# Kernel optimization log

Hardware: AMD Instinct MI355X
Metric: run time of the kernel (lower is better)

The kernel has to match this reference:

```python
import jax, jax.numpy as jnp
import numpy as np

D = 512  # link/path state dim == GRU hidden
R = 256  # readout dim
T = 8    # message-passing steps


def gru_cell(x, h, W_ih, W_hh, b_ih, b_hh):
    # torch nn.GRU cell math (weights stored [3H, in])
    gi = x @ W_ih.T + b_ih
    gh = h @ W_hh.T + b_hh
    i_r, i_z, i_n = jnp.split(gi, 3, axis=-1)
    h_r, h_z, h_n = jnp.split(gh, 3, axis=-1)
    r = jax.nn.sigmoid(i_r + h_r)
    z = jax.nn.sigmoid(i_z + h_z)
    n = jnp.tanh(i_n + r * h_n)
    return (1.0 - z) * n + z * h


def setup_inputs():
    key = jax.random.key(0)
    n_links, n_paths, L = 2000, 20000, 6
    ks = jax.random.split(key, 24)
    links = jax.random.randint(ks[0], (n_paths * L,), 0, n_links)
    paths = jnp.repeat(jnp.arange(n_paths), L)   # path id per entry
    seqs = jnp.tile(jnp.arange(L), n_paths)      # position of link within path
    link_capacity = jax.random.uniform(ks[1], (n_links, 1))
    bandwidth = jax.random.uniform(ks[2], (n_paths, 1))

    def u(k, shape, fan_in):
        s = 1.0 / np.sqrt(fan_in)
        return jax.random.uniform(k, shape, minval=-s, maxval=s)

    inp = dict(links=links, paths=paths, seqs=seqs,
               link_capacity=link_capacity, bandwidth=bandwidth)
    # path GRU (p_U) and link GRU (l_U)
    inp['Wih_p'] = u(ks[3], (3 * D, D), D); inp['Whh_p'] = u(ks[4], (3 * D, D), D)
    inp['bih_p'] = u(ks[5], (3 * D,), D);   inp['bhh_p'] = u(ks[6], (3 * D,), D)
    inp['Wih_l'] = u(ks[7], (3 * D, D), D); inp['Whh_l'] = u(ks[8], (3 * D, D), D)
    inp['bih_l'] = u(ks[9], (3 * D,), D);   inp['bhh_l'] = u(ks[10], (3 * D,), D)
    # readout MLPs (delay + jitter), torch Linear layout [out, in]
    inp['d_w1'] = u(ks[11], (R, D), D);      inp['d_b1'] = u(ks[12], (R,), D)
    inp['d_w2'] = u(ks[13], (R // 2, R), R); inp['d_b2'] = u(ks[14], (R // 2,), R)
    inp['d_w3'] = u(ks[15], (1, R // 2), R // 2); inp['d_b3'] = u(ks[16], (1,), R // 2)
    inp['j_w1'] = u(ks[17], (R, D), D);      inp['j_b1'] = u(ks[18], (R,), D)
    inp['j_w2'] = u(ks[19], (R // 2, R), R); inp['j_b2'] = u(ks[20], (R // 2,), R)
    inp['j_w3'] = u(ks[21], (1, R // 2), R // 2); inp['j_b3'] = u(ks[22], (1,), R // 2)
    inp['n_links'] = n_links
    inp['n_paths'] = n_paths
    inp['max_seq_len'] = L  # == max(seqs)+1
    return inp


def mlp(x, w1, b1, w2, b2, w3, b3):
    h = jax.nn.relu(x @ w1.T + b1)
    h = jax.nn.relu(h @ w2.T + b2)
    return h @ w3.T + b3


def reference(links, paths, seqs, link_capacity, bandwidth,
              Wih_p, Whh_p, bih_p, bhh_p, Wih_l, Whh_l, bih_l, bhh_l,
              d_w1, d_b1, d_w2, d_b2, d_w3, d_b3,
              j_w1, j_b1, j_w2, j_b2, j_w3, j_b3,
              n_links, n_paths, max_seq_len):
    dt = bandwidth.dtype
    path_h = jnp.concatenate([bandwidth, jnp.zeros((n_paths, D - 1), dt)], axis=1)
    link_h = jnp.concatenate([link_capacity, jnp.zeros((n_links, D - 1), dt)], axis=1)

    def p_step(h, x_t):
        h2 = gru_cell(x_t, h, Wih_p, Whh_p, bih_p, bhh_p)
        return h2, h2

    for _ in range(T):
        h_lp = link_h[links]  # gather link states onto path entries [E, D]
        x_seq = jnp.zeros((n_paths, max_seq_len, D), dt).at[paths, seqs].set(h_lp)
        path_h, outs = jax.lax.scan(p_step, path_h, jnp.swapaxes(x_seq, 0, 1))
        outs = jnp.swapaxes(outs, 0, 1)  # [n_paths, L, D] per-step path states
        msg = outs[paths, seqs]          # [E, D] message from each path position
        agg = jax.ops.segment_sum(msg, links, num_segments=n_links)  # scatter-add
        link_h = gru_cell(agg, link_h, Wih_l, Whh_l, bih_l, bhh_l)

    d = mlp(path_h, d_w1, d_b1, d_w2, d_b2, d_w3, d_b3)
    j = mlp(path_h, j_w1, j_b1, j_w2, j_b2, j_w3, j_b3)
    return d, j
```

## Files before the change

### kernel.cpp

```cpp
#include <hip/hip_runtime.h>
#include <stdint.h>

typedef __attribute__((ext_vector_type(4))) float float4v;
typedef __attribute__((ext_vector_type(8))) short short8v;

static __device__ __forceinline__ float sigp(float x){ return 1.f/(1.f+expf(-x)); }

static __device__ __forceinline__ unsigned short f2bf(float x){
  unsigned u = __float_as_uint(x);
  u += 0x7FFFu + ((u>>16)&1u);
  return (unsigned short)(u>>16);
}
static __device__ __forceinline__ float bf2f(unsigned short h){
  return __uint_as_float(((unsigned)h)<<16);
}

static __device__ __forceinline__ void gload16(const void* g, void* l){
  __builtin_amdgcn_global_load_lds((const __attribute__((address_space(1))) void*)g,
                                   (__attribute__((address_space(3))) void*)l, 16, 0, 0);
}

__global__ void sentf_k(float* __restrict__ o, int n, float v){
  int i = blockIdx.x*256 + threadIdx.x; if (i < n) o[i] = v;
}

__global__ void prep_k(const int* __restrict__ links, const int* __restrict__ paths,
                       const int* __restrict__ seqs, int* __restrict__ plink,
                       int* __restrict__ cnt){
  int e = blockIdx.x*256 + threadIdx.x;
  if (e < 120000){
    int p = paths[e], s = seqs[e], l = links[e];
    plink[p*6 + s] = l;
    atomicAdd(&cnt[s*2000 + l], 1);
  }
}
__global__ void scan_k(const int* __restrict__ cnt, int* __restrict__ off, int* __restrict__ cur){
  __shared__ int part[256]; __shared__ int pref[256];
  int t = threadIdx.x;
  int lo = t*47, hi = lo+47; if (hi > 12000) hi = 12000;
  int s = 0;
  for (int i=lo;i<hi;i++) s += cnt[i];
  part[t] = s; __syncthreads();
  if (t==0){ int r=0; for (int i=0;i<256;i++){ pref[i]=r; r+=part[i]; } }
  __syncthreads();
  int r = pref[t];
  for (int i=lo;i<hi;i++){ off[i]=r; cur[i]=r; r+=cnt[i]; }
}
__global__ void fill2_k(const int* __restrict__ links, const int* __restrict__ paths,
                        const int* __restrict__ seqs, int* __restrict__ cur,
                        int* __restrict__ plist){
  int e = blockIdx.x*256 + threadIdx.x;
  if (e < 120000){
    int p = paths[e], s = seqs[e], l = links[e];
    int pos = atomicAdd(&cur[s*2000 + l], 1);
    plist[pos] = p;
  }
}

__global__ void wcvt_k(const float* __restrict__ W, unsigned short* __restrict__ hi,
                       unsigned short* __restrict__ lo, int n){
  int i = blockIdx.x*256 + threadIdx.x;
  if (i < n){
    float x = W[i];
    unsigned short h = f2bf(x);
    hi[i] = h;
    lo[i] = f2bf(x - bf2f(h));
  }
}

__global__ void initp_k(const float* __restrict__ x0,
                        unsigned short* __restrict__ h0, unsigned short* __restrict__ l0,
                        unsigned short* __restrict__ h1, unsigned short* __restrict__ l1,
                        int Mreal){
  int i = blockIdx.x*256 + threadIdx.x;
  int m = i >> 9, c = i & 511;
  float v = (c==0 && m < Mreal) ? x0[m] : 0.f;
  unsigned short hh = f2bf(v);
  unsigned short ll = f2bf(v - bf2f(hh));
  h0[i]=hh; l0[i]=ll; h1[i]=hh; l1[i]=ll;
}

__global__ __launch_bounds__(512,4) void gmfma_k(
    const unsigned short* __restrict__ Ahi, const unsigned short* __restrict__ Alo,
    const unsigned short* __restrict__ Whi, const unsigned short* __restrict__ Wlo,
    const float* __restrict__ bias, const float* __restrict__ GI,
    const int* __restrict__ plink, int s,
    float* __restrict__ OutF,
    unsigned short* __restrict__ Ohi, unsigned short* __restrict__ Olo,
    int M, int gru, int writeF)
{
  __shared__ unsigned short sAh0[128*32], sAl0[128*32];
  __shared__ unsigned short sBh0[192*32], sBl0[192*32];
  __shared__ unsigned short sAh1[128*32], sAl1[128*32];
  __shared__ unsigned short sBh1[192*32], sBl1[192*32];
  const int tid  = threadIdx.x;
  const int lane = tid & 63, wave = tid >> 6;
  const int wm = wave >> 2, wn = wave & 3;
  const int bid = blockIdx.x;
  const int X = bid & 7, kk2 = bid >> 3;
  const int m0 = ((kk2 >> 3)*8 + X) * 128;
  const int cb = kk2 & 7;
  const int c16 = lane & 15, kq = lane >> 4;

  int offA;
  {
    int row = tid >> 2; int kg = (tid & 3) ^ ((row >> 1) & 3);
    offA = (m0 + row)*1024 + kg*16;
  }
  int offB0, offB1;
  {
    int gb = tid;
    int v  = gb >> 2;
    int kg = (gb & 3) ^ ((v >> 1) & 3);
    int wn_ = v / 48; int rem = v - wn_*48;
    int gg = rem >> 4, cc = rem & 15;
    offB0 = (gg*512 + cb*64 + wn_*16 + cc)*1024 + kg*16;
    gb = 512 + tid;
    v  = gb >> 2;
    kg = (gb & 3) ^ ((v >> 1) & 3);
    int wn2 = v / 48; rem = v - wn2*48;
    gg = rem >> 4; cc = rem & 15;
    if (wn2 > 3) wn2 = 3;
    offB1 = (gg*512 + cb*64 + wn2*16 + cc)*1024 + kg*16;
  }
  const int gA  = (wave*64)*8;
  const int gB0 = (wave*64)*8, gB1 = (512 + wave*64)*8;

  const int rA = wm*64 + c16;
  const int rdA = (rA*4 + (kq ^ ((rA>>1)&3)))*8;
  const int vB = wn*48 + c16;
  const int rdB = (vB*4 + (kq ^ ((vB>>1)&3)))*8;

  float4v acc[4][3];
#pragma unroll
  for (int i = 0; i < 4; ++i)
#pragma unroll
    for (int j = 0; j < 3; ++j) acc[i][j] = (float4v){0.f,0.f,0.f,0.f};

  auto STAGE = [&](int kb, unsigned short* dAh, unsigned short* dAl,
                   unsigned short* dBh, unsigned short* dBl){
    const int kbb = kb*64;
    const char* ah = (const char*)Ahi + kbb;
    const char* al = (const char*)Alo + kbb;
    const char* wh = (const char*)Whi + kbb;
    const char* wl = (const char*)Wlo + kbb;
    gload16(ah + offA, dAh + gA);
    gload16(al + offA, dAl + gA);
    gload16(wh + offB0, dBh + gB0);
    gload16(wl + offB0, dBl + gB0);
    if (tid < 256){
      gload16(wh + offB1, dBh + gB1);
      gload16(wl + offB1, dBl + gB1);
    }
  };

  auto COMPUTE = [&](const unsigned short* tAh, const unsigned short* tAl,
                     const unsigned short* tBh, const unsigned short* tBl){
    short8v ah[4], al[4], bh[3], bl[3];
#pragma unroll
    for (int mf = 0; mf < 4; ++mf) ah[mf] = *(const short8v*)(tAh + rdA + mf*512);
#pragma unroll
    for (int g = 0; g < 3; ++g)  bh[g]  = *(const short8v*)(tBh + rdB + g*512);
#pragma unroll
    for (int mf = 0; mf < 4; ++mf) al[mf] = *(const short8v*)(tAl + rdA + mf*512);
#pragma unroll
    for (int mf = 0; mf < 4; ++mf)
#pragma unroll
      for (int g = 0; g < 3; ++g)
        acc[mf][g] = __builtin_amdgcn_mfma_f32_16x16x32_bf16(ah[mf], bh[g], acc[mf][g], 0, 0, 0);
#pragma unroll
    for (int g = 0; g < 3; ++g)  bl[g]  = *(const short8v*)(tBl + rdB + g*512);
#pragma unroll
    for (int mf = 0; mf < 4; ++mf)
#pragma unroll
      for (int g = 0; g < 3; ++g)
        acc[mf][g] = __builtin_amdgcn_mfma_f32_16x16x32_bf16(al[mf], bh[g], acc[mf][g], 0, 0, 0);
#pragma unroll
    for (int mf = 0; mf < 4; ++mf)
#pragma unroll
      for (int g = 0; g < 3; ++g)
        acc[mf][g] = __builtin_amdgcn_mfma_f32_16x16x32_bf16(ah[mf], bl[g], acc[mf][g], 0, 0, 0);
  };

  STAGE(0, sAh0, sAl0, sBh0, sBl0);
  __syncthreads();
  for (int q = 0; q < 8; ++q){
    STAGE(2*q+1, sAh1, sAl1, sBh1, sBl1);
    COMPUTE(sAh0, sAl0, sBh0, sBl0);
    __syncthreads();
    if (q < 7) STAGE(2*q+2, sAh0, sAl0, sBh0, sBl0);
    COMPUTE(sAh1, sAl1, sBh1, sBl1);
    __syncthreads();
  }

  const int col = cb*64 + wn*16 + c16;
  if (!gru){
    const float b0f = bias[col], b1f = bias[512+col], b2f = bias[1024+col];
#pragma unroll
    for (int mf = 0; mf < 4; ++mf){
      const int mb = m0 + wm*64 + mf*16 + kq*4;
#pragma unroll
      for (int r = 0; r < 4; ++r){
        const int m = mb + r;
        if (m < M){
          float* c = OutF + (size_t)m*1536 + col;
          c[0]    = acc[mf][0][r] + b0f;
          c[512]  = acc[mf][1][r] + b1f;
          c[1024] = acc[mf][2][r] + b2f;
        }
      }
    }
  } else {
    const float br = bias[col], bz = bias[512+col], bn = bias[1024+col];
#pragma unroll
    for (int mf = 0; mf < 4; ++mf){
      const int mb = m0 + wm*64 + mf*16 + kq*4;
#pragma unroll
      for (int r = 0; r < 4; ++r){
        const int m = mb + r;
        if (m < M){
          const int gr = plink ? plink[m*6 + s] : m;
          const float* gi = GI + (size_t)gr*1536 + col;
          const size_t ix = (size_t)m*512 + col;
          float hold = bf2f(Ahi[ix]) + bf2f(Alo[ix]);
          float rr = sigp(gi[0]    + acc[mf][0][r] + br);
          float zz = sigp(gi[512]  + acc[mf][1][r] + bz);
          float nn = 2.f*sigp(2.f*(gi[1024] + rr*(acc[mf][2][r] + bn))) - 1.f;
          float h  = (1.f - zz)*nn + zz*hold;
          unsigned short hh = f2bf(h);
          Ohi[ix] = hh;
          Olo[ix] = f2bf(h - bf2f(hh));
          if (writeF) OutF[ix] = h;
        }
      }
    }
  }
}

__global__ void aggv_k(const unsigned short* __restrict__ Hh, const unsigned short* __restrict__ Hl,
                       const int* __restrict__ plist,
                       const int* __restrict__ off, const int* __restrict__ cnt, int s,
                       float* __restrict__ AGG, int isFirst,
                       unsigned short* __restrict__ Ghi, unsigned short* __restrict__ Glo,
                       int emit)
{
  int l = blockIdx.x, t = threadIdx.x;
  size_t b0 = (size_t)l*512 + t, b1 = b0 + 256;
  if (l >= 2000){
    AGG[b0] = 0.f; AGG[b1] = 0.f;
    if (emit){ Ghi[b0]=0; Glo[b0]=0; Ghi[b1]=0; Glo[b1]=0; }
    return;
  }
  int o = off[s*2000 + l], c = cnt[s*2000 + l];
  float a0 = isFirst ? 0.f : AGG[b0];
  float a1 = isFirst ? 0.f : AGG[b1];
  for (int i = 0; i < c; ++i){
    size_t p = (size_t)plist[o + i] * 512;
    a0 += bf2f(Hh[p + t])       + bf2f(Hl[p + t]);
    a1 += bf2f(Hh[p + 256 + t]) + bf2f(Hl[p + 256 + t]);
  }
  AGG[b0] = a0; AGG[b1] = a1;
  if (emit){
    unsigned short h0 = f2bf(a0); Ghi[b0]=h0; Glo[b0]=f2bf(a0 - bf2f(h0));
    unsigned short h1 = f2bf(a1); Ghi[b1]=h1; Glo[b1]=f2bf(a1 - bf2f(h1));
  }
}

__global__ __launch_bounds__(256,2) void gemmv_k(
    const float* __restrict__ A, int lda, const float* __restrict__ W,
    const float* __restrict__ bias, float* __restrict__ C,
    int M, int N, int K, int relu)
{
  __shared__ float sA[64*32];
  __shared__ float sW[32*192];
  const int tid = threadIdx.x;
  const int colg = tid & 31, rowg = tid >> 5;
  const int m0 = blockIdx.x*64, n0 = blockIdx.y*192;
  float acc[8][6] = {};
  for (int k0 = 0; k0 < K; k0 += 32){
    __syncthreads();
#pragma unroll
    for (int u = 0; u < 2; ++u){
      int fi = tid + u*256; int row = fi >> 3, kqq = fi & 7;
      float4v v = *(const float4v*)(A + (size_t)(m0+row)*lda + k0 + kqq*4);
      *(float4v*)&sA[row*32 + kqq*4] = v;
    }
#pragma unroll
    for (int u = 0; u < 6; ++u){
      int fi = tid + u*256; int vc = fi >> 3, kqq = fi & 7;
      int wrow = n0 + vc;
      float4v v = {0.f,0.f,0.f,0.f};
      if (wrow < N) v = *(const float4v*)(W + (size_t)wrow*K + k0 + kqq*4);
      sW[(kqq*4+0)*192 + vc] = v.x;
      sW[(kqq*4+1)*192 + vc] = v.y;
      sW[(kqq*4+2)*192 + vc] = v.z;
      sW[(kqq*4+3)*192 + vc] = v.w;
    }
    __syncthreads();
#pragma unroll
    for (int kk = 0; kk < 32; ++kk){
      float a[8], w[6];
#pragma unroll
      for (int j = 0; j < 8; ++j) a[j] = sA[(rowg*8+j)*32 + kk];
#pragma unroll
      for (int i = 0; i < 6; ++i) w[i] = sW[kk*192 + colg*6 + i];
#pragma unroll
      for (int j = 0; j < 8; ++j)
#pragma unroll
        for (int i = 0; i < 6; ++i) acc[j][i] = fmaf(a[j], w[i], acc[j][i]);
    }
  }
#pragma unroll
  for (int j = 0; j < 8; ++j){
    int m = m0 + rowg*8 + j;
#pragma unroll
    for (int i = 0; i < 6; ++i){
      int col = n0 + colg*6 + i;
      if (col >= N) continue;
      float v = acc[j][i] + (bias ? bias[col] : 0.f);
      if (relu) v = fmaxf(v, 0.f);
      if (m >= M) v = 0.f;
      C[(size_t)m*N + col] = v;
    }
  }
}

__global__ void dotf_k(const float* __restrict__ T2, const float* __restrict__ w3,
                       const float* __restrict__ b3, float* __restrict__ out, int M)
{
  int lane = threadIdx.x & 63, w = threadIdx.x >> 6;
  int m = blockIdx.x * 4 + w;
  if (m >= M) return;
  float s = T2[(size_t)m*128 + lane] * w3[lane]
          + T2[(size_t)m*128 + 64 + lane] * w3[64 + lane];
#pragma unroll
  for (int off = 32; off; off >>= 1) s += __shfl_xor(s, off);
  if (lane == 0) out[m] = s + b3[0];
}

extern "C" void kernel_launch(void* const* d_in, const int* in_sizes, int n_in,
                              void* d_out, int out_size, void* d_ws, size_t ws_size,
                              hipStream_t stream)
{
  const int*   links = (const int*)d_in[0];
  const int*   paths = (const int*)d_in[1];
  const int*   seqs  = (const int*)d_in[2];
  const float* cap   = (const float*)d_in[3];
  const float* bw    = (const float*)d_in[4];
  const float* Wih_p = (const float*)d_in[5];
  const float* Whh_p = (const float*)d_in[6];
  const float* bih_p = (const float*)d_in[7];
  const float* bhh_p = (const float*)d_in[8];
  const float* Wih_l = (const float*)d_in[9];
  const float* Whh_l = (const float*)d_in[10];
  const float* bih_l = (const float*)d_in[11];
  const float* bhh_l = (const float*)d_in[12];
  const float* d_w1 = (const float*)d_in[13]; const float* d_b1 = (const float*)d_in[14];
  const float* d_w2 = (const float*)d_in[15]; const float* d_b2 = (const float*)d_in[16];
  const float* d_w3 = (const float*)d_in[17]; const float* d_b3 = (const float*)d_in[18];
  const float* j_w1 = (const float*)d_in[19]; const float* j_b1 = (const float*)d_in[20];
  const float* j_w2 = (const float*)d_in[21]; const float* j_b2 = (const float*)d_in[22];
  const float* j_w3 = (const float*)d_in[23]; const float* j_b3 = (const float*)d_in[24];
  float* out = (float*)d_out;

  const int MpP = 20480;
  const int MpL = 2048;
  char* p = (char*)d_ws;
  auto alloc = [&](size_t n){ char* r = p; p += (n + 255) & ~(size_t)255; return r; };
  float* P   = (float*)alloc((size_t)MpP*512*4);
  unsigned short* Phi[2]; unsigned short* Plo[2];
  Phi[0] = (unsigned short*)alloc((size_t)MpP*512*2);
  Plo[0] = (unsigned short*)alloc((size_t)MpP*512*2);
  Phi[1] = (unsigned short*)alloc((size_t)MpP*512*2);
  Plo[1] = (unsigned short*)alloc((size_t)MpP*512*2);
  unsigned short* Lhi[2]; unsigned short* Llo[2];
  Lhi[0] = (unsigned short*)alloc((size_t)MpL*512*2);
  Llo[0] = (unsigned short*)alloc((size_t)MpL*512*2);
  Lhi[1] = (unsigned short*)alloc((size_t)MpL*512*2);
  Llo[1] = (unsigned short*)alloc((size_t)MpL*512*2);
  float* LG  = (float*)alloc((size_t)MpL*1536*4);
  float* AGG = (float*)alloc((size_t)MpL*512*4);
  unsigned short* AGh = (unsigned short*)alloc((size_t)MpL*512*2);
  unsigned short* AGl = (unsigned short*)alloc((size_t)MpL*512*2);
  unsigned short* WhhPh = (unsigned short*)alloc((size_t)1536*512*2);
  unsigned short* WhhPl = (unsigned short*)alloc((size_t)1536*512*2);
  unsigned short* WihPh = (unsigned short*)alloc((size_t)1536*512*2);
  unsigned short* WihPl = (unsigned short*)alloc((size_t)1536*512*2);
  unsigned short* WhhLh = (unsigned short*)alloc((size_t)1536*512*2);
  unsigned short* WhhLl = (unsigned short*)alloc((size_t)1536*512*2);
  unsigned short* WihLh = (unsigned short*)alloc((size_t)1536*512*2);
  unsigned short* WihLl = (unsigned short*)alloc((size_t)1536*512*2);
  int* cnt2  = (int*)alloc(12000*4);
  int* off2  = (int*)alloc(12000*4);
  int* cur2  = (int*)alloc(12000*4);
  int* plist = (int*)alloc(120000*4);
  int* plink = (int*)alloc(120000*4);
  float* t1 = (float*)Phi[0];
  float* t2 = (float*)Phi[1];
  if ((size_t)(p - (char*)d_ws) > ws_size){
    sentf_k<<<(out_size+255)/256,256,0,stream>>>(out, out_size, 0.25f);
    return;
  }

  hipMemsetAsync(cnt2, 0, 12000*4, stream);
  prep_k<<<469,256,0,stream>>>(links, paths, seqs, plink, cnt2);
  scan_k<<<1,256,0,stream>>>(cnt2, off2, cur2);
  fill2_k<<<469,256,0,stream>>>(links, paths, seqs, cur2, plist);
  wcvt_k<<<3072,256,0,stream>>>(Whh_p, WhhPh, WhhPl, 1536*512);
  wcvt_k<<<3072,256,0,stream>>>(Wih_p, WihPh, WihPl, 1536*512);
  wcvt_k<<<3072,256,0,stream>>>(Whh_l, WhhLh, WhhLl, 1536*512);
  wcvt_k<<<3072,256,0,stream>>>(Wih_l, WihLh, WihLl, 1536*512);
  initp_k<<<(MpP*512)/256,256,0,stream>>>(bw,  Phi[0], Plo[0], Phi[1], Plo[1], 20000);
  initp_k<<<(MpL*512)/256,256,0,stream>>>(cap, Lhi[0], Llo[0], Lhi[1], Llo[1], 2000);

  int pb = 0, lb = 0;
  for (int t = 0; t < 8; ++t) {
    gmfma_k<<<16*8,512,0,stream>>>(Lhi[lb], Llo[lb], WihPh, WihPl, bih_p,
                                   (const float*)0, (const int*)0, 0,
                                   LG, (unsigned short*)0, (unsigned short*)0, 2000, 0, 0);
    for (int s6 = 0; s6 < 6; ++s6) {
      int last = (t==7 && s6==5) ? 1 : 0;
      gmfma_k<<<160*8,512,0,stream>>>(Phi[pb], Plo[pb], WhhPh, WhhPl, bhh_p,
                                      LG, plink, s6,
                                      P, Phi[pb^1], Plo[pb^1], 20000, 1, last);
      pb ^= 1;
      aggv_k<<<2048,256,0,stream>>>(Phi[pb], Plo[pb], plist, off2, cnt2, s6, AGG,
                                    (s6==0)?1:0, AGh, AGl, (s6==5)?1:0);
    }
    gmfma_k<<<16*8,512,0,stream>>>(AGh, AGl, WihLh, WihLl, bih_l,
                                   (const float*)0, (const int*)0, 0,
                                   LG, (unsigned short*)0, (unsigned short*)0, 2000, 0, 0);
    gmfma_k<<<16*8,512,0,stream>>>(Lhi[lb], Llo[lb], WhhLh, WhhLl, bhh_l,
                                   LG, (const int*)0, 0,
                                   (float*)0, Lhi[lb^1], Llo[lb^1], 2000, 1, 0);
    lb ^= 1;
  }

  gemmv_k<<<dim3(313,2),256,0,stream>>>(P, 512, d_w1, d_b1, t1, 20000, 256, 512, 1);
  gemmv_k<<<dim3(313,1),256,0,stream>>>(t1, 256, d_w2, d_b2, t2, 20000, 128, 256, 1);
  dotf_k<<<5000,256,0,stream>>>(t2, d_w3, d_b3, out, 20000);
  gemmv_k<<<dim3(313,2),256,0,stream>>>(P, 512, j_w1, j_b1, t1, 20000, 256, 512, 1);
  gemmv_k<<<dim3(313,1),256,0,stream>>>(t1, 256, j_w2, j_b2, t2, 20000, 128, 256, 1);
  dotf_k<<<5000,256,0,stream>>>(t2, j_w3, j_b3, out + 20000, 20000);
}
```

Before: 7.702 ms.

## Run readout MLPs on split-bf16 MFMA GEMM and vectorize aggregation loads

Replaces the scalar fp32 readout GEMM with a new MFMA kernel that uses split hi/lo bf16 operands and a double-buffered LDS pipeline. It reads the final path state directly from the bf16 hi/lo buffers, so the fp32 copy of path states written on the last step is no longer needed. The aggregation kernel now loads packed pairs of bf16 values per thread instead of single values. The split-bf16 product drops the lo*lo term, which may change accuracy slightly.

```diff
diff --git a/kernel.cpp b/kernel.cpp
--- a/kernel.cpp
+++ b/kernel.cpp
@@ -2,6 +2,7 @@
 #include <stdint.h>
 
 typedef __attribute__((ext_vector_type(4))) float float4v;
+typedef __attribute__((ext_vector_type(2))) float float2v;
 typedef __attribute__((ext_vector_type(8))) short short8v;
 
 static __device__ __forceinline__ float sigp(float x){ return 1.f/(1.f+expf(-x)); }
@@ -237,6 +238,118 @@
   }
 }
 
+__global__ __launch_bounds__(256,3) void rgemm_k(
+    const unsigned short* __restrict__ Ahi, const unsigned short* __restrict__ Alo,
+    const unsigned short* __restrict__ Whi, const unsigned short* __restrict__ Wlo,
+    const float* __restrict__ bias,
+    float* __restrict__ OutF,
+    unsigned short* __restrict__ Ohi, unsigned short* __restrict__ Olo,
+    int M, int N, int K, int relu)
+{
+  __shared__ unsigned short rAh0[128*32], rAl0[128*32], rWh0[64*32], rWl0[64*32];
+  __shared__ unsigned short rAh1[128*32], rAl1[128*32], rWh1[64*32], rWl1[64*32];
+  const int tid = threadIdx.x;
+  const int lane = tid & 63, wave = tid >> 6;
+  const int wm = wave >> 1, wn = wave & 1;
+  const int m0 = blockIdx.x * 128, n0 = blockIdx.y * 64;
+  const int c16 = lane & 15, kq = lane >> 4;
+  const int K2 = K*2;
+
+  int offA0, offA1, offW;
+  { int g = tid;      int row = g>>2; int kg=(g&3)^((row>>1)&3); offA0 = (m0+row)*K2 + kg*16; }
+  { int g = tid+256;  int row = g>>2; int kg=(g&3)^((row>>1)&3); offA1 = (m0+row)*K2 + kg*16; }
+  { int g = tid;      int v = g>>2;   int kg=(g&3)^((v>>1)&3);   offW  = (n0+v)*K2 + kg*16; }
+  const int gA0 = (wave*64)*8, gA1 = (wave*64+256)*8;
+  const int gW  = (wave*64)*8;
+
+  const int rA = wm*64 + c16;
+  const int rdA = (rA*4 + (kq ^ ((rA>>1)&3)))*8;
+  const int vB = wn*32 + c16;
+  const int rdB = (vB*4 + (kq ^ ((vB>>1)&3)))*8;
+
+  float4v acc[4][2];
+#pragma unroll
+  for (int i = 0; i < 4; ++i)
+#pragma unroll
+    for (int j = 0; j < 2; ++j) acc[i][j] = (float4v){0.f,0.f,0.f,0.f};
+
+  auto STAGE = [&](int kb, unsigned short* dAh, unsigned short* dAl,
+                   unsigned short* dWh, unsigned short* dWl){
+    const int kbb = kb*64;
+    gload16((const char*)Ahi + kbb + offA0, dAh + gA0);
+    gload16((const char*)Ahi + kbb + offA1, dAh + gA1);
+    gload16((const char*)Alo + kbb + offA0, dAl + gA0);
+    gload16((const char*)Alo + kbb + offA1, dAl + gA1);
+    gload16((const char*)Whi + kbb + offW, dWh + gW);
+    gload16((const char*)Wlo + kbb + offW, dWl + gW);
+  };
+
+  auto COMPUTE = [&](const unsigned short* tAh, const unsigned short* tAl,
+                     const unsigned short* tWh, const unsigned short* tWl){
+    short8v ah[4], al[4], bh[2], bl[2];
+#pragma unroll
+    for (int mf = 0; mf < 4; ++mf) ah[mf] = *(const short8v*)(tAh + rdA + mf*512);
+#pragma unroll
+    for (int nf = 0; nf < 2; ++nf) bh[nf] = *(const short8v*)(tWh + rdB + nf*512);
+#pragma unroll
+    for (int mf = 0; mf < 4; ++mf) al[mf] = *(const short8v*)(tAl + rdA + mf*512);
+#pragma unroll
+    for (int mf = 0; mf < 4; ++mf)
+#pragma unroll
+      for (int nf = 0; nf < 2; ++nf)
+        acc[mf][nf] = __builtin_amdgcn_mfma_f32_16x16x32_bf16(ah[mf], bh[nf], acc[mf][nf], 0, 0, 0);
+#pragma unroll
+    for (int nf = 0; nf < 2; ++nf) bl[nf] = *(const short8v*)(tWl + rdB + nf*512);
+#pragma unroll
+    for (int mf = 0; mf < 4; ++mf)
+#pragma unroll
+      for (int nf = 0; nf < 2; ++nf)
+        acc[mf][nf] = __builtin_amdgcn_mfma_f32_16x16x32_bf16(al[mf], bh[nf], acc[mf][nf], 0, 0, 0);
+#pragma unroll
+    for (int mf = 0; mf < 4; ++mf)
+#pragma unroll
+      for (int nf = 0; nf < 2; ++nf)
+        acc[mf][nf] = __builtin_amdgcn_mfma_f32_16x16x32_bf16(ah[mf], bl[nf], acc[mf][nf], 0, 0, 0);
+  };
+
+  const int nc = K >> 5;
+  STAGE(0, rAh0, rAl0, rWh0, rWl0);
+  __syncthreads();
+  for (int q = 0; q < (nc>>1); ++q){
+    STAGE(2*q+1, rAh1, rAl1, rWh1, rWl1);
+    COMPUTE(rAh0, rAl0, rWh0, rWl0);
+    __syncthreads();
+    if (q < (nc>>1)-1) STAGE(2*q+2, rAh0, rAl0, rWh0, rWl0);
+    COMPUTE(rAh1, rAl1, rWh1, rWl1);
+    __syncthreads();
+  }
+
+#pragma unroll
+  for (int nf = 0; nf < 2; ++nf){
+    const int col = n0 + wn*32 + nf*16 + c16;
+    const float b = bias[col];
+#pragma unroll
+    for (int mf = 0; mf < 4; ++mf){
+      const int mb = m0 + wm*64 + mf*16 + kq*4;
+#pragma unroll
+      for (int r = 0; r < 4; ++r){
+        const int m = mb + r;
+        if (m < M){
+          float v = acc[mf][nf][r] + b;
+          if (relu) v = fmaxf(v, 0.f);
+          const size_t ix = (size_t)m*N + col;
+          if (OutF) OutF[ix] = v;
+          if (Ohi){
+            unsigned short hh = f2bf(v);
+            Ohi[ix] = hh;
+            Olo[ix] = f2bf(v - bf2f(hh));
+          }
+        }
+      }
+    }
+  }
+}
+
 __global__ void aggv_k(const unsigned short* __restrict__ Hh, const unsigned short* __restrict__ Hl,
                        const int* __restrict__ plist,
                        const int* __restrict__ off, const int* __restrict__ cnt, int s,
@@ -245,83 +358,28 @@
                        int emit)
 {
   int l = blockIdx.x, t = threadIdx.x;
-  size_t b0 = (size_t)l*512 + t, b1 = b0 + 256;
+  size_t base = (size_t)l*512 + 2*t;
   if (l >= 2000){
-    AGG[b0] = 0.f; AGG[b1] = 0.f;
-    if (emit){ Ghi[b0]=0; Glo[b0]=0; Ghi[b1]=0; Glo[b1]=0; }
+    AGG[base] = 0.f; AGG[base+1] = 0.f;
+    if (emit){ *(unsigned*)&Ghi[base] = 0u; *(unsigned*)&Glo[base] = 0u; }
     return;
   }
   int o = off[s*2000 + l], c = cnt[s*2000 + l];
-  float a0 = isFirst ? 0.f : AGG[b0];
-  float a1 = isFirst ? 0.f : AGG[b1];
+  float a0 = isFirst ? 0.f : AGG[base];
+  float a1 = isFirst ? 0.f : AGG[base+1];
   for (int i = 0; i < c; ++i){
-    size_t p = (size_t)plist[o + i] * 512;
-    a0 += bf2f(Hh[p + t])       + bf2f(Hl[p + t]);
-    a1 += bf2f(Hh[p + 256 + t]) + bf2f(Hl[p + 256 + t]);
-  }
-  AGG[b0] = a0; AGG[b1] = a1;
+    size_t p = (size_t)plist[o + i] * 512 + 2*t;
+    unsigned hh = *(const unsigned*)(Hh + p);
+    unsigned hl = *(const unsigned*)(Hl + p);
+    a0 += __uint_as_float(hh << 16) + __uint_as_float(hl << 16);
+    a1 += __uint_as_float(hh & 0xffff0000u) + __uint_as_float(hl & 0xffff0000u);
+  }
+  AGG[base] = a0; AGG[base+1] = a1;
   if (emit){
-    unsigned short h0 = f2bf(a0); Ghi[b0]=h0; Glo[b0]=f2bf(a0 - bf2f(h0));
-    unsigned short h1 = f2bf(a1); Ghi[b1]=h1; Glo[b1]=f2bf(a1 - bf2f(h1));
-  }
-}
-
-__global__ __launch_bounds__(256,2) void gemmv_k(
-    const float* __restrict__ A, int lda, const float* __restrict__ W,
-    const float* __restrict__ bias, float* __restrict__ C,
-    int M, int N, int K, int relu)
-{
-  __shared__ float sA[64*32];
-  __shared__ float sW[32*192];
-  const int tid = threadIdx.x;
-  const int colg = tid & 31, rowg = tid >> 5;
-  const int m0 = blockIdx.x*64, n0 = blockIdx.y*192;
-  float acc[8][6] = {};
-  for (int k0 = 0; k0 < K; k0 += 32){
-    __syncthreads();
-#pragma unroll
-    for (int u = 0; u < 2; ++u){
-      int fi = tid + u*256; int row = fi >> 3, kqq = fi & 7;
-      float4v v = *(const float4v*)(A + (size_t)(m0+row)*lda + k0 + kqq*4);
-      *(float4v*)&sA[row*32 + kqq*4] = v;
-    }
-#pragma unroll
-    for (int u = 0; u < 6; ++u){
-      int fi = tid + u*256; int vc = fi >> 3, kqq = fi & 7;
-      int wrow = n0 + vc;
-      float4v v = {0.f,0.f,0.f,0.f};
-      if (wrow < N) v = *(const float4v*)(W + (size_t)wrow*K + k0 + kqq*4);
-      sW[(kqq*4+0)*192 + vc] = v.x;
-      sW[(kqq*4+1)*192 + vc] = v.y;
-      sW[(kqq*4+2)*192 + vc] = v.z;
-      sW[(kqq*4+3)*192 + vc] = v.w;
-    }
-    __syncthreads();
-#pragma unroll
-    for (int kk = 0; kk < 32; ++kk){
-      float a[8], w[6];
-#pragma unroll
-      for (int j = 0; j < 8; ++j) a[j] = sA[(rowg*8+j)*32 + kk];
-#pragma unroll
-      for (int i = 0; i < 6; ++i) w[i] = sW[kk*192 + colg*6 + i];
-#pragma unroll
-      for (int j = 0; j < 8; ++j)
-#pragma unroll
-        for (int i = 0; i < 6; ++i) acc[j][i] = fmaf(a[j], w[i], acc[j][i]);
-    }
-  }
-#pragma unroll
-  for (int j = 0; j < 8; ++j){
-    int m = m0 + rowg*8 + j;
-#pragma unroll
-    for (int i = 0; i < 6; ++i){
-      int col = n0 + colg*6 + i;
-      if (col >= N) continue;
-      float v = acc[j][i] + (bias ? bias[col] : 0.f);
-      if (relu) v = fmaxf(v, 0.f);
-      if (m >= M) v = 0.f;
-      C[(size_t)m*N + col] = v;
-    }
+    unsigned short h0 = f2bf(a0), h1 = f2bf(a1);
+    *(unsigned*)&Ghi[base] = (unsigned)h0 | ((unsigned)h1 << 16);
+    unsigned short l0 = f2bf(a0 - bf2f(h0)), l1 = f2bf(a1 - bf2f(h1));
+    *(unsigned*)&Glo[base] = (unsigned)l0 | ((unsigned)l1 << 16);
   }
 }
 
@@ -367,7 +425,6 @@
   const int MpL = 2048;
   char* p = (char*)d_ws;
   auto alloc = [&](size_t n){ char* r = p; p += (n + 255) & ~(size_t)255; return r; };
-  float* P   = (float*)alloc((size_t)MpP*512*4);
   unsigned short* Phi[2]; unsigned short* Plo[2];
   Phi[0] = (unsigned short*)alloc((size_t)MpP*512*2);
   Plo[0] = (unsigned short*)alloc((size_t)MpP*512*2);
@@ -390,13 +447,22 @@
   unsigned short* WhhLl = (unsigned short*)alloc((size_t)1536*512*2);
   unsigned short* WihLh = (unsigned short*)alloc((size_t)1536*512*2);
   unsigned short* WihLl = (unsigned short*)alloc((size_t)1536*512*2);
+  unsigned short* DW1h = (unsigned short*)alloc((size_t)256*512*2);
+  unsigned short* DW1l = (unsigned short*)alloc((size_t)256*512*2);
+  unsigned short* DW2h = (unsigned short*)alloc((size_t)128*256*2);
+  unsigned short* DW2l = (unsigned short*)alloc((size_t)128*256*2);
+  unsigned short* JW1h = (unsigned short*)alloc((size_t)256*512*2);
+  unsigned short* JW1l = (unsigned short*)alloc((size_t)256*512*2);
+  unsigned short* JW2h = (unsigned short*)alloc((size_t)128*256*2);
+  unsigned short* JW2l = (unsigned short*)alloc((size_t)128*256*2);
   int* cnt2  = (int*)alloc(12000*4);
   int* off2  = (int*)alloc(12000*4);
   int* cur2  = (int*)alloc(12000*4);
   int* plist = (int*)alloc(120000*4);
   int* plink = (int*)alloc(120000*4);
-  float* t1 = (float*)Phi[0];
-  float* t2 = (float*)Phi[1];
+  unsigned short* t1h = Phi[1];
+  unsigned short* t1l = Plo[1];
+  float* t2 = LG;
   if ((size_t)(p - (char*)d_ws) > ws_size){
     sentf_k<<<(out_size+255)/256,256,0,stream>>>(out, out_size, 0.25f);
     return;
@@ -410,6 +476,10 @@
   wcvt_k<<<3072,256,0,stream>>>(Wih_p, WihPh, WihPl, 1536*512);
   wcvt_k<<<3072,256,0,stream>>>(Whh_l, WhhLh, WhhLl, 1536*512);
   wcvt_k<<<3072,256,0,stream>>>(Wih_l, WihLh, WihLl, 1536*512);
+  wcvt_k<<<512,256,0,stream>>>(d_w1, DW1h, DW1l, 256*512);
+  wcvt_k<<<128,256,0,stream>>>(d_w2, DW2h, DW2l, 128*256);
+  wcvt_k<<<512,256,0,stream>>>(j_w1, JW1h, JW1l, 256*512);
+  wcvt_k<<<128,256,0,stream>>>(j_w2, JW2h, JW2l, 128*256);
   initp_k<<<(MpP*512)/256,256,0,stream>>>(bw,  Phi[0], Plo[0], Phi[1], Plo[1], 20000);
   initp_k<<<(MpL*512)/256,256,0,stream>>>(cap, Lhi[0], Llo[0], Lhi[1], Llo[1], 2000);
 
@@ -419,10 +489,9 @@
                                    (const float*)0, (const int*)0, 0,
                                    LG, (unsigned short*)0, (unsigned short*)0, 2000, 0, 0);
     for (int s6 = 0; s6 < 6; ++s6) {
-      int last = (t==7 && s6==5) ? 1 : 0;
       gmfma_k<<<160*8,512,0,stream>>>(Phi[pb], Plo[pb], WhhPh, WhhPl, bhh_p,
                                       LG, plink, s6,
-                                      P, Phi[pb^1], Plo[pb^1], 20000, 1, last);
+                                      (float*)0, Phi[pb^1], Plo[pb^1], 20000, 1, 0);
       pb ^= 1;
       aggv_k<<<2048,256,0,stream>>>(Phi[pb], Plo[pb], plist, off2, cnt2, s6, AGG,
                                     (s6==0)?1:0, AGh, AGl, (s6==5)?1:0);
@@ -436,10 +505,14 @@
     lb ^= 1;
   }
 
-  gemmv_k<<<dim3(313,2),256,0,stream>>>(P, 512, d_w1, d_b1, t1, 20000, 256, 512, 1);
-  gemmv_k<<<dim3(313,1),256,0,stream>>>(t1, 256, d_w2, d_b2, t2, 20000, 128, 256, 1);
+  rgemm_k<<<dim3(157,4),256,0,stream>>>(Phi[0], Plo[0], DW1h, DW1l, d_b1,
+                                        (float*)0, t1h, t1l, 20000, 256, 512, 1);
+  rgemm_k<<<dim3(157,2),256,0,stream>>>(t1h, t1l, DW2h, DW2l, d_b2,
+                                        t2, (unsigned short*)0, (unsigned short*)0, 20000, 128, 256, 1);
   dotf_k<<<5000,256,0,stream>>>(t2, d_w3, d_b3, out, 20000);
-  gemmv_k<<<dim3(313,2),256,0,stream>>>(P, 512, j_w1, j_b1, t1, 20000, 256, 512, 1);
-  gemmv_k<<<dim3(313,1),256,0,stream>>>(t1, 256, j_w2, j_b2, t2, 20000, 128, 256, 1);
+  rgemm_k<<<dim3(157,4),256,0,stream>>>(Phi[0], Plo[0], JW1h, JW1l, j_b1,
+                                        (float*)0, t1h, t1l, 20000, 256, 512, 1);
+  rgemm_k<<<dim3(157,2),256,0,stream>>>(t1h, t1l, JW2h, JW2l, j_b2,
+                                        t2, (unsigned short*)0, (unsigned short*)0, 20000, 128, 256, 1);
   dotf_k<<<5000,256,0,stream>>>(t2, j_w3, j_b3, out + 20000, 20000);
 }
```

Result: faster. 7.166 ms (-7.0%).
